# Kernel tuning notes

Hardware: AMD Instinct MI355X
Metric: run time of the kernel (lower is better)

The kernel has to match this reference:

```python
import jax, jax.numpy as jnp
from jax import lax
import numpy as np

CHUNK = 64      # chunk_size init kwarg
MAX_LOG = 20.0  # clamp bound used in ssd()
DT_BIAS = 0.01
NEG_SLOPE = 0.01  # torch LeakyReLU default


def segsum(a):
    """a: (..., T) -> (..., T, T); ss[i,j] = sum_{k=j+1..i} a[k], -inf above diag."""
    T = a.shape[-1]
    rep = jnp.broadcast_to(a[..., :, None], a.shape + (T,))
    strict_lower = jnp.tril(jnp.ones((T, T), dtype=bool), -1)
    ss = jnp.cumsum(jnp.where(strict_lower, rep, 0.0), axis=-2)
    keep = jnp.tril(jnp.ones((T, T), dtype=bool), 0)
    return jnp.where(keep, ss, -jnp.inf)


def setup_inputs() -> dict:
    key = jax.random.key(0)
    ks = jax.random.split(key, 7)
    T, B, S, F = 4096, 4, 16, 64   # time, batch, spatial heads, in_channels
    N, P, K = 16, 64, 5            # state_dim, head_dim, conv_size
    CH = 2 * N + P + 1             # bc_conv out channels = 97
    return {
        "x": jax.random.normal(ks[0], (T, B, S, F), dtype=jnp.float32),
        "conv_w": jax.random.normal(ks[1], (CH, F, K), dtype=jnp.float32) * 0.05,
        "conv_b": jax.random.normal(ks[2], (CH,), dtype=jnp.float32) * 0.05,
        "pass_w": jax.random.normal(ks[3], (1, F), dtype=jnp.float32) * 0.1,
        "pass_b": jax.random.normal(ks[4], (1,), dtype=jnp.float32) * 0.1,
        "red_w": jax.random.normal(ks[5], (1, P), dtype=jnp.float32) * 0.1,
        "red_b": jax.random.normal(ks[6], (1,), dtype=jnp.float32) * 0.1,
        "dt_param": jnp.zeros((1,), dtype=jnp.float32),  # torch init [0.0]
    }


def _forward(x, conv_w, conv_b, pass_w, pass_b, red_w, red_b, dt_param):
    T, B, S, F = x.shape
    CH, _, K = conv_w.shape
    P = red_w.shape[1]
    N = (CH - P - 1) // 2
    c = T // CHUNK

    # ---- _compute_ssm_params (parallel mode, causal left-pad) ----
    xr = jnp.moveaxis(x.reshape(T, B * S, F), 0, 2)          # (bs, F, T)
    xp = jnp.pad(xr, ((0, 0), (0, 0), (K - 1, 0)))           # left pad context
    bcax = lax.conv_general_dilated(
        xp, conv_w, window_strides=(1,), padding="VALID",
        dimension_numbers=("NCH", "OIH", "NCH")) + conv_b[None, :, None]
    bcax = jax.nn.sigmoid(bcax) + bcax                        # (bs, CH, T)
    bcax = bcax.reshape(B, S, CH, T)
    Bm = bcax[:, :, :N, :]                                    # (b,s,n,t)
    Cm = bcax[:, :, N:2 * N, :]                               # (b,s,n,t)
    A = -jnp.abs(bcax[:, :, 2 * N, :])                        # (b,s,t)
    Xc = bcax[:, :, 2 * N + 1:, :]                            # (b,s,p,t)
    dt = jax.nn.softplus(dt_param)[0] + DT_BIAS
    lAd = dt * A                                              # (b,s,t)
    Bd = Bm * ((jnp.exp(lAd) - 1.0) / (A + 1e-9))[:, :, None, :]
    Dx = x @ pass_w[0] + pass_b[0]                            # (t,b,s) passthrough

    # ---- ssd: chunked Mamba-2 scan ----
    Xb = jnp.moveaxis(Xc, 3, 0).swapaxes(0, 1).reshape(B, c, CHUNK, S, P)
    Bb = jnp.moveaxis(Bd, 3, 0).swapaxes(0, 1).reshape(B, c, CHUNK, S, N)
    Cb = jnp.moveaxis(Cm, 3, 0).swapaxes(0, 1).reshape(B, c, CHUNK, S, N)
    Ab = lAd.reshape(B, S, c, CHUNK)                          # (b,s,c,l)
    A_cumsum = jnp.cumsum(Ab, axis=-1)                        # (b,s,c,l)

    L = jnp.exp(jnp.clip(segsum(Ab), -MAX_LOG, MAX_LOG))      # (b,s,c,l,l)
    Y_diag = jnp.einsum("bclsn,bcmsn,bsclm,bcmsp->bclsp", Cb, Bb, L, Xb)

    decay_states = jnp.exp(jnp.clip(A_cumsum[..., -1:] - A_cumsum, -MAX_LOG, MAX_LOG))
    states = jnp.einsum("bclsn,bscl,bclsp->bcspn", Bb, decay_states, Xb)
    states = jnp.concatenate([jnp.zeros_like(states[:, :1]), states], axis=1)

    A_last = jnp.pad(A_cumsum[..., -1], ((0, 0), (0, 0), (1, 0)))  # (b,s,c+1)
    decay_chunk = jnp.exp(jnp.clip(segsum(A_last), -MAX_LOG, MAX_LOG))
    new_states = jnp.einsum("bszc,bcspn->bzspn", decay_chunk, states)
    states_c = new_states[:, :-1]                             # (b,c,s,p,n)

    state_decay_out = jnp.exp(A_cumsum)                       # (b,s,c,l), no clamp (as in source)
    Y_off = jnp.einsum("bclsn,bcspn,bscl->bclsp", Cb, states_c, state_decay_out)

    Y = (Y_diag + Y_off).reshape(B, T, S, P).swapaxes(0, 1)   # (t,b,s,p)

    # ---- reduce + leaky-relu passthrough ----
    y = Y @ red_w[0] + red_b[0]                               # (t,b,s)
    return y + jnp.where(Dx >= 0, Dx, NEG_SLOPE * Dx)


def reference(x, conv_w, conv_b, pass_w, pass_b, red_w, red_b, dt_param):
    return _forward(x, conv_w, conv_b, pass_w, pass_b, red_w, red_b, dt_param)
```

## Files before the change

### kernel.cpp

```cpp
#include <hip/hip_runtime.h>
#include <hip/hip_bf16.h>
#include <math.h>


#define Tn 4096
#define BSn 64
#define Fn 64
#define CHn 97
#define CHP 112
#define Kn 5
#define NCn 64

typedef __attribute__((ext_vector_type(8))) short bf16x8;
typedef __attribute__((ext_vector_type(4))) float f32x4;

static __device__ __forceinline__ unsigned short f2bf(float v) {
    __hip_bfloat16 b = __float2bfloat16(v);
    return *reinterpret_cast<unsigned short*>(&b);
}
static __device__ __forceinline__ float bf2f(unsigned short u) {
    unsigned v = ((unsigned)u) << 16;
    return __builtin_bit_cast(float, v);
}
static __device__ __forceinline__ float bflo(unsigned u) {
    return __builtin_bit_cast(float, u << 16);
}
static __device__ __forceinline__ float bfhi(unsigned u) {
    return __builtin_bit_cast(float, u & 0xffff0000u);
}

#define OFF_BD   0
#define OFF_CM   (OFF_BD + 4194304)
#define OFF_LAD  (OFF_CM + 4194304)
#define OFF_XQ   (OFF_LAD + 262144)
#define OFF_DL   (OFF_XQ + 262144)
#define OFF_ACS  (OFF_DL + 262144)
#define OFF_SRED (OFF_ACS + 262144)
#define OFF_CSUM (OFF_SRED + 65536)
#define OFF_SNS  (OFF_CSUM + 4096)
#define OFF_WBH  (OFF_SNS + 65536)
#define OFF_WBL  (OFF_WBH + 17920)

__global__ __launch_bounds__(256) void k_prep(const float* __restrict__ conv_w,
                                              const float* __restrict__ pass_w,
                                              unsigned short* __restrict__ wbh,
                                              unsigned short* __restrict__ wbl) {
    int idx = blockIdx.x * 256 + threadIdx.x;
    if (idx >= Kn * CHP * Fn) return;
    int f = idx & 63;
    int rest = idx >> 6;
    int ch = rest % CHP;
    int k = rest / CHP;
    float w = 0.f;
    if (ch < CHn) w = conv_w[(ch * Fn + f) * Kn + k];
    else if (ch == 97 && k == 4) w = pass_w[f];
    unsigned short hi = f2bf(w);
    wbh[idx] = hi;
    if (ch >= 32 && ch < 48)
        wbl[(k * 16 + (ch - 32)) * 64 + f] = f2bf(w - bf2f(hi));
}

__global__ __launch_bounds__(256) void k_fwd(
    const float* __restrict__ x, const unsigned short* __restrict__ wbh,
    const unsigned short* __restrict__ wbl,
    const float* __restrict__ conv_b, const float* __restrict__ pass_b,
    const float* __restrict__ red_w, const float* __restrict__ red_b,
    const float* __restrict__ dtp,
    unsigned short* __restrict__ Cm_h, float* __restrict__ Acs_ws,
    float* __restrict__ yp_ws, float* __restrict__ sred_ws,
    float* __restrict__ csum_ws) {
    const int wgid = blockIdx.x;
    const int seq = wgid >> 3;
    const int bs = seq & 63;
    const int ci = ((seq >> 6) << 3) | (wgid & 7);
    const int tid = threadIdx.x;
    const int wv = tid >> 6, lane = tid & 63;
    const int qd = lane >> 4, n = lane & 15;

    __shared__ alignas(16) unsigned char pool[19584];
    unsigned short* xsb = (unsigned short*)pool;
    unsigned short* xlo = (unsigned short*)(pool + 9792);
    float* B0  = (float*)pool;
    float* Ct  = (float*)(pool + 5120);
    float* pxl = (float*)(pool + 10240);
    float* px2 = (float*)(pool + 11264);
    float* zsh = (float*)(pool + 12288);
    float* dl  = (float*)(pool + 12544);

    const int tB = (wv == 3) ? 6 : wv + 4;
    const unsigned short* pBw = (wv == 2) ? wbl : wbh;
    const int sB = (wv == 2) ? 16 : CHP;
    const int cB = (wv == 2) ? 0 : 16 * tB;
    bf16x8 wA[10], wB[10];
#pragma unroll
    for (int s = 0; s < 10; ++s) {
        const int k = s >> 1, f0 = 32 * (s & 1) + qd * 8;
        wA[s] = *(const bf16x8*)&wbh[((k * CHP + 16 * wv + n) << 6) + f0];
        wB[s] = *(const bf16x8*)&pBw[((k * sB + cB + n) << 6) + f0];
    }

    float4 v[5];
#pragma unroll
    for (int it = 0; it < 5; ++it) {
        int idx = tid + it * 256;
        int tt = idx >> 4, fq = (idx & 15) * 4;
        int t = ci * 64 - 4 + tt;
        v[it] = (idx < 68 * 16 && t >= 0)
                    ? *(const float4*)&x[(t * 64 + bs) * 64 + fq]
                    : make_float4(0.f, 0.f, 0.f, 0.f);
    }
#pragma unroll
    for (int it = 0; it < 5; ++it) {
        int idx = tid + it * 256;
        if (idx < 68 * 16) {
            int tt = idx >> 4, fq = (idx & 15) * 4;
            ushort4 h, lo;
            h.x = f2bf(v[it].x); lo.x = f2bf(v[it].x - bf2f(h.x));
            h.y = f2bf(v[it].y); lo.y = f2bf(v[it].y - bf2f(h.y));
            h.z = f2bf(v[it].z); lo.z = f2bf(v[it].z - bf2f(h.z));
            h.w = f2bf(v[it].w); lo.w = f2bf(v[it].w - bf2f(h.w));
            *(ushort4*)&xsb[tt * 72 + fq] = h;
            *(ushort4*)&xlo[tt * 72 + fq] = lo;
        }
    }
    __syncthreads();

    f32x4 accA[4], accB[4];
#pragma unroll
    for (int rg = 0; rg < 4; ++rg) {
        accA[rg] = (f32x4){0.f, 0.f, 0.f, 0.f};
        accB[rg] = (f32x4){0.f, 0.f, 0.f, 0.f};
    }
    if (wv == 2) {
#pragma unroll
        for (int s = 0; s < 10; ++s) {
            const int k = s >> 1, f0 = 32 * (s & 1) + qd * 8;
#pragma unroll
            for (int rg = 0; rg < 4; ++rg) {
                bf16x8 av = *(const bf16x8*)&xsb[(16 * rg + n + k) * 72 + f0];
                bf16x8 al = *(const bf16x8*)&xlo[(16 * rg + n + k) * 72 + f0];
                accA[rg] = __builtin_amdgcn_mfma_f32_16x16x32_bf16(av, wA[s], accA[rg], 0, 0, 0);
                accA[rg] = __builtin_amdgcn_mfma_f32_16x16x32_bf16(al, wA[s], accA[rg], 0, 0, 0);
                accA[rg] = __builtin_amdgcn_mfma_f32_16x16x32_bf16(av, wB[s], accA[rg], 0, 0, 0);
            }
        }
    } else {
#pragma unroll
        for (int s = 0; s < 10; ++s) {
            const int k = s >> 1, f0 = 32 * (s & 1) + qd * 8;
#pragma unroll
            for (int rg = 0; rg < 4; ++rg) {
                bf16x8 av = *(const bf16x8*)&xsb[(16 * rg + n + k) * 72 + f0];
                accA[rg] = __builtin_amdgcn_mfma_f32_16x16x32_bf16(av, wA[s], accA[rg], 0, 0, 0);
                accB[rg] = __builtin_amdgcn_mfma_f32_16x16x32_bf16(av, wB[s], accB[rg], 0, 0, 0);
            }
        }
    }
    __syncthreads();

    const int cbase = (bs * 64 + ci) * 64;
    float px[4][4];
#pragma unroll
    for (int rg = 0; rg < 4; ++rg)
#pragma unroll
        for (int reg = 0; reg < 4; ++reg) px[rg][reg] = 0.f;

    if (wv == 0) {
        const float cb0 = conv_b[n];
        const float cb4 = conv_b[64 + n], rw4 = red_w[31 + n];
#pragma unroll
        for (int rg = 0; rg < 4; ++rg)
#pragma unroll
            for (int reg = 0; reg < 4; ++reg) {
                int row = 16 * rg + 4 * qd + reg;
                float z0 = accA[rg][reg] + cb0;
                float a0 = z0 + 1.f / (1.f + __expf(-z0));
                accA[rg][reg] = a0;
                B0[row * 20 + n] = a0;
                float z4 = accB[rg][reg] + cb4;
                px[rg][reg] = (z4 + 1.f / (1.f + __expf(-z4))) * rw4;
            }
    } else if (wv == 1) {
        const float cb1 = conv_b[16 + n];
        const float cb5 = conv_b[80 + n], rw5 = red_w[47 + n];
#pragma unroll
        for (int rg = 0; rg < 4; ++rg)
#pragma unroll
            for (int reg = 0; reg < 4; ++reg) {
                int row = 16 * rg + 4 * qd + reg;
                float z1 = accA[rg][reg] + cb1;
                float a1 = z1 + 1.f / (1.f + __expf(-z1));
                Ct[row * 20 + n] = a1;
                Cm_h[(cbase + row) * 16 + n] = f2bf(a1);
                float z5 = accB[rg][reg] + cb5;
                px[rg][reg] = (z5 + 1.f / (1.f + __expf(-z5))) * rw5;
            }
    } else if (wv == 2) {
        const float cb2 = conv_b[32 + n];
        const float rw2 = (n >= 1) ? red_w[n - 1] : 0.f;
#pragma unroll
        for (int rg = 0; rg < 4; ++rg)
#pragma unroll
            for (int reg = 0; reg < 4; ++reg) {
                int row = 16 * rg + 4 * qd + reg;
                if (n == 0) zsh[row] = accA[rg][reg];
                float z = accA[rg][reg] + cb2;
                px[rg][reg] = (z + 1.f / (1.f + __expf(-z))) * rw2;
            }
    } else {
        const float cb3 = conv_b[48 + n], rw3 = red_w[15 + n];
        const float cb6 = conv_b[96], rw6 = red_w[63];
        const float pb = pass_b[0], rb = red_b[0];
#pragma unroll
        for (int rg = 0; rg < 4; ++rg)
#pragma unroll
            for (int reg = 0; reg < 4; ++reg) {
                int row = 16 * rg + 4 * qd + reg;
                float z3 = accA[rg][reg] + cb3;
                px[rg][reg] = (z3 + 1.f / (1.f + __expf(-z3))) * rw3;
                if (n == 0) {
                    float z6 = accB[rg][reg] + cb6;
                    px[rg][reg] += (z6 + 1.f / (1.f + __expf(-z6))) * rw6;
                }
                if (n == 1) {
                    float Dx = accB[rg][reg] + pb;
                    float DL = (Dx >= 0.f) ? Dx : 0.01f * Dx;
                    dl[row] = DL + rb;
                }
            }
    }
#pragma unroll
    for (int m = 1; m < 16; m <<= 1)
#pragma unroll
        for (int rg = 0; rg < 4; ++rg)
#pragma unroll
            for (int reg = 0; reg < 4; ++reg)
                px[rg][reg] += __shfl_xor(px[rg][reg], m, 64);
    if (n == 0)
#pragma unroll
        for (int rg = 0; rg < 4; ++rg)
#pragma unroll
            for (int reg = 0; reg < 4; ++reg)
                pxl[wv * 64 + 16 * rg + 4 * qd + reg] = px[rg][reg];
    __syncthreads();

    const int l = lane;
    const float dt = log1pf(expf(dtp[0])) + 0.01f;
    float zA = zsh[l] + conv_b[32];
    float aA = zA + 1.f / (1.f + __expf(-zA));
    float An = -fabsf(aA);
    float lAd = dt * An;
    float fac = (__expf(lAd) - 1.f) / (An + 1e-9f);
    float s = lAd;
#pragma unroll
    for (int k = 1; k < 64; k <<= 1) {
        float t = __shfl_up(s, k, 64);
        if (l >= k) s += t;
    }
    const float acs_l = s;
    const float tot = __shfl(s, 63, 64);
    float xq = pxl[0 * 64 + l] + pxl[1 * 64 + l] + pxl[2 * 64 + l] + pxl[3 * 64 + l];
    const float wd = fac * xq;
    const float wsd = wd * __expf(fmaxf(tot - acs_l, -20.f));
    if (wv == 3) {
        Acs_ws[bs * Tn + ci * 64 + l] = acs_l;
        if (l == 0) csum_ws[bs * 64 + ci] = tot;
    }

    const float4 cc0 = *(const float4*)&Ct[l * 20 + 0];
    const float4 cc1 = *(const float4*)&Ct[l * 20 + 4];
    const float4 cc2 = *(const float4*)&Ct[l * 20 + 8];
    const float4 cc3 = *(const float4*)&Ct[l * 20 + 12];
    float part = 0.f;
#pragma unroll
    for (int mm = 0; mm < 16; ++mm) {
        const int m = 16 * wv + mm;
        const float4 b0 = *(const float4*)&B0[m * 20 + 0];
        const float4 b1 = *(const float4*)&B0[m * 20 + 4];
        const float4 b2 = *(const float4*)&B0[m * 20 + 8];
        const float4 b3 = *(const float4*)&B0[m * 20 + 12];
        float g = cc0.x * b0.x + cc0.y * b0.y + cc0.z * b0.z + cc0.w * b0.w +
                  cc1.x * b1.x + cc1.y * b1.y + cc1.z * b1.z + cc1.w * b1.w +
                  cc2.x * b2.x + cc2.y * b2.y + cc2.z * b2.z + cc2.w * b2.w +
                  cc3.x * b3.x + cc3.y * b3.y + cc3.z * b3.z + cc3.w * b3.w;
        float am = __shfl(acs_l, m, 64);
        float wm = __shfl(wd, m, 64);
        float arg = (m <= l) ? fmaxf(acs_l - am, -20.f) : -20.f;
        part += __expf(arg) * g * wm;
    }
    px2[wv * 64 + l] = part;

    if (wv == 0) {
        float sp = 0.f;
#pragma unroll
        for (int rg = 0; rg < 4; ++rg)
#pragma unroll
            for (int reg = 0; reg < 4; ++reg)
                sp += accA[rg][reg] * __shfl(wsd, 16 * rg + 4 * qd + reg, 64);
        sp += __shfl_xor(sp, 16, 64);
        sp += __shfl_xor(sp, 32, 64);
        if (l < 16) sred_ws[(bs * 64 + ci) * 16 + l] = sp;
    }
    __syncthreads();

    if (wv == 0)
        yp_ws[bs * Tn + ci * 64 + l] =
            px2[0 * 64 + l] + px2[1 * 64 + l] + px2[2 * 64 + l] + px2[3 * 64 + l] + dl[l];
}

__global__ __launch_bounds__(256) void k_out(
    const unsigned short* __restrict__ Cm_h, const float* __restrict__ Acs_ws,
    const float* __restrict__ sred_ws, const float* __restrict__ csum_ws,
    const float* __restrict__ yp_ws, float* __restrict__ out) {
    const int bs = blockIdx.y;
    const int tid = threadIdx.x;
    const int wv = tid >> 6, l = tid & 63;
    const int ci = blockIdx.x * 4 + wv;
    __shared__ float sn[4][16];
    const int base = bs * Tn + ci * 64;

    const float dexp = __expf(csum_ws[bs * 64 + l]);
#pragma unroll
    for (int j = 0; j < 4; ++j) {
        const int n = 4 * wv + j;
        float s = sred_ws[(bs * 64 + l) * 16 + n];
        float d = dexp;
#pragma unroll
        for (int k = 1; k < 64; k <<= 1) {
            float dp = __shfl_up(d, k, 64);
            float sp = __shfl_up(s, k, 64);
            if (l >= k) {
                s = d * sp + s;
                d = d * dp;
            }
        }
        float se = __shfl_up(s, 1, 64);
        float sns = (l == 0) ? 0.f : se;
        if ((l >> 2) == blockIdx.x) sn[l & 3][n] = sns;
    }

    const unsigned short* crow = &Cm_h[((bs * 64 + ci) * 64 + l) * 16];
    uint4 ua = *(const uint4*)crow;
    uint4 ub = *(const uint4*)(crow + 8);
    float yp = yp_ws[base + l];
    float acl = Acs_ws[base + l];
    __syncthreads();

    const float* s = sn[wv];
    float go = bflo(ua.x) * s[0]  + bfhi(ua.x) * s[1] +
               bflo(ua.y) * s[2]  + bfhi(ua.y) * s[3] +
               bflo(ua.z) * s[4]  + bfhi(ua.z) * s[5] +
               bflo(ua.w) * s[6]  + bfhi(ua.w) * s[7] +
               bflo(ub.x) * s[8]  + bfhi(ub.x) * s[9] +
               bflo(ub.y) * s[10] + bfhi(ub.y) * s[11] +
               bflo(ub.z) * s[12] + bfhi(ub.z) * s[13] +
               bflo(ub.w) * s[14] + bfhi(ub.w) * s[15];
    out[(ci * 64 + l) * 64 + bs] = yp + __expf(acl) * go;
}

extern "C" void kernel_launch(void* const* d_in, const int* in_sizes, int n_in,
                              void* d_out, int out_size, void* d_ws,
                              size_t ws_size, hipStream_t stream) {
    const float* x = (const float*)d_in[0];
    const float* conv_w = (const float*)d_in[1];
    const float* conv_b = (const float*)d_in[2];
    const float* pass_w = (const float*)d_in[3];
    const float* pass_b = (const float*)d_in[4];
    const float* red_w = (const float*)d_in[5];
    const float* red_b = (const float*)d_in[6];
    const float* dtp = (const float*)d_in[7];
    float* out = (float*)d_out;
    float* W = (float*)d_ws;
    (void)in_sizes; (void)n_in; (void)out_size; (void)ws_size;

    unsigned short* Cm_h = (unsigned short*)(W + OFF_CM);
    float* yp_ws = W + OFF_DL;
    float* Acs_ws = W + OFF_ACS;
    float* sred_ws = W + OFF_SRED;
    float* csum_ws = W + OFF_CSUM;
    unsigned short* wbh = (unsigned short*)(W + OFF_WBH);
    unsigned short* wbl = (unsigned short*)(W + OFF_WBL);

    k_prep<<<dim3((Kn * CHP * Fn + 255) / 256), dim3(256), 0, stream>>>(
        conv_w, pass_w, wbh, wbl);
    k_fwd<<<dim3(NCn * BSn), dim3(256), 0, stream>>>(
        x, wbh, wbl, conv_b, pass_b, red_w, red_b, dtp,
        Cm_h, Acs_ws, yp_ws, sred_ws, csum_ws);
    k_out<<<dim3(NCn / 4, BSn), dim3(256), 0, stream>>>(
        Cm_h, Acs_ws, sred_ws, csum_ws, yp_ws, out);
}
```

Measured before the change: 199.6 us.

## Make k_fwd persistent over 8 tiles with register prefetch of next x tile

The forward kernel now launches 512 blocks, and each loops over 8 consecutive (bs, chunk) tiles instead of launching one block per tile. Each block loads its weight fragments into registers once and reuses them across the 8 tiles. It also issues the global loads for the next tile's x slice right after the MFMA stage, so they overlap with the epilogue math. The cost is fewer blocks, which lowers occupancy and latency hiding, and an extra barrier per tile. The tile-to-block mapping also changes from the old interleaved ordering to contiguous bs runs, which can affect L2 reuse of the overlapping x halos.

```diff
diff --git a/kernel.cpp b/kernel.cpp
--- a/kernel.cpp
+++ b/kernel.cpp
@@ -10,6 +10,8 @@
 #define CHP 112
 #define Kn 5
 #define NCn 64
+#define NBLK 512
+#define TPB 8
 
 typedef __attribute__((ext_vector_type(8))) short bf16x8;
 typedef __attribute__((ext_vector_type(4))) float f32x4;
@@ -69,10 +71,7 @@
     unsigned short* __restrict__ Cm_h, float* __restrict__ Acs_ws,
     float* __restrict__ yp_ws, float* __restrict__ sred_ws,
     float* __restrict__ csum_ws) {
-    const int wgid = blockIdx.x;
-    const int seq = wgid >> 3;
-    const int bs = seq & 63;
-    const int ci = ((seq >> 6) << 3) | (wgid & 7);
+    const int b = blockIdx.x;
     const int tid = threadIdx.x;
     const int wv = tid >> 6, lane = tid & 63;
     const int qd = lane >> 4, n = lane & 15;
@@ -99,213 +98,239 @@
         wB[s] = *(const bf16x8*)&pBw[((k * sB + cB + n) << 6) + f0];
     }
 
+    const float dt = log1pf(expf(dtp[0])) + 0.01f;
+
     float4 v[5];
-#pragma unroll
-    for (int it = 0; it < 5; ++it) {
-        int idx = tid + it * 256;
-        int tt = idx >> 4, fq = (idx & 15) * 4;
-        int t = ci * 64 - 4 + tt;
-        v[it] = (idx < 68 * 16 && t >= 0)
-                    ? *(const float4*)&x[(t * 64 + bs) * 64 + fq]
-                    : make_float4(0.f, 0.f, 0.f, 0.f);
+    {
+        const int t0 = b * TPB;
+        const int bs = t0 & 63, ci = t0 >> 6;
+#pragma unroll
+        for (int it = 0; it < 5; ++it) {
+            int idx = tid + it * 256;
+            int tt = idx >> 4, fq = (idx & 15) * 4;
+            int t = ci * 64 - 4 + tt;
+            v[it] = (idx < 68 * 16 && t >= 0)
+                        ? *(const float4*)&x[(t * 64 + bs) * 64 + fq]
+                        : make_float4(0.f, 0.f, 0.f, 0.f);
+        }
     }
-#pragma unroll
-    for (int it = 0; it < 5; ++it) {
-        int idx = tid + it * 256;
-        if (idx < 68 * 16) {
-            int tt = idx >> 4, fq = (idx & 15) * 4;
-            ushort4 h, lo;
-            h.x = f2bf(v[it].x); lo.x = f2bf(v[it].x - bf2f(h.x));
-            h.y = f2bf(v[it].y); lo.y = f2bf(v[it].y - bf2f(h.y));
-            h.z = f2bf(v[it].z); lo.z = f2bf(v[it].z - bf2f(h.z));
-            h.w = f2bf(v[it].w); lo.w = f2bf(v[it].w - bf2f(h.w));
-            *(ushort4*)&xsb[tt * 72 + fq] = h;
-            *(ushort4*)&xlo[tt * 72 + fq] = lo;
-        }
+
+    for (int it8 = 0; it8 < TPB; ++it8) {
+        const int tt8 = b * TPB + it8;
+        const int bs = tt8 & 63, ci = tt8 >> 6;
+
+#pragma unroll
+        for (int it = 0; it < 5; ++it) {
+            int idx = tid + it * 256;
+            if (idx < 68 * 16) {
+                int tt = idx >> 4, fq = (idx & 15) * 4;
+                ushort4 h, lo;
+                h.x = f2bf(v[it].x); lo.x = f2bf(v[it].x - bf2f(h.x));
+                h.y = f2bf(v[it].y); lo.y = f2bf(v[it].y - bf2f(h.y));
+                h.z = f2bf(v[it].z); lo.z = f2bf(v[it].z - bf2f(h.z));
+                h.w = f2bf(v[it].w); lo.w = f2bf(v[it].w - bf2f(h.w));
+                *(ushort4*)&xsb[tt * 72 + fq] = h;
+                *(ushort4*)&xlo[tt * 72 + fq] = lo;
+            }
+        }
+        __syncthreads();
+
+        f32x4 accA[4], accB[4];
+#pragma unroll
+        for (int rg = 0; rg < 4; ++rg) {
+            accA[rg] = (f32x4){0.f, 0.f, 0.f, 0.f};
+            accB[rg] = (f32x4){0.f, 0.f, 0.f, 0.f};
+        }
+        if (wv == 2) {
+#pragma unroll
+            for (int s = 0; s < 10; ++s) {
+                const int k = s >> 1, f0 = 32 * (s & 1) + qd * 8;
+#pragma unroll
+                for (int rg = 0; rg < 4; ++rg) {
+                    bf16x8 av = *(const bf16x8*)&xsb[(16 * rg + n + k) * 72 + f0];
+                    bf16x8 al = *(const bf16x8*)&xlo[(16 * rg + n + k) * 72 + f0];
+                    accA[rg] = __builtin_amdgcn_mfma_f32_16x16x32_bf16(av, wA[s], accA[rg], 0, 0, 0);
+                    accA[rg] = __builtin_amdgcn_mfma_f32_16x16x32_bf16(al, wA[s], accA[rg], 0, 0, 0);
+                    accA[rg] = __builtin_amdgcn_mfma_f32_16x16x32_bf16(av, wB[s], accA[rg], 0, 0, 0);
+                }
+            }
+        } else {
+#pragma unroll
+            for (int s = 0; s < 10; ++s) {
+                const int k = s >> 1, f0 = 32 * (s & 1) + qd * 8;
+#pragma unroll
+                for (int rg = 0; rg < 4; ++rg) {
+                    bf16x8 av = *(const bf16x8*)&xsb[(16 * rg + n + k) * 72 + f0];
+                    accA[rg] = __builtin_amdgcn_mfma_f32_16x16x32_bf16(av, wA[s], accA[rg], 0, 0, 0);
+                    accB[rg] = __builtin_amdgcn_mfma_f32_16x16x32_bf16(av, wB[s], accB[rg], 0, 0, 0);
+                }
+            }
+        }
+        __syncthreads();
+
+        if (it8 + 1 < TPB) {
+            const int tn = tt8 + 1;
+            const int bsN = tn & 63, ciN = tn >> 6;
+#pragma unroll
+            for (int it = 0; it < 5; ++it) {
+                int idx = tid + it * 256;
+                int tt = idx >> 4, fq = (idx & 15) * 4;
+                int t = ciN * 64 - 4 + tt;
+                v[it] = (idx < 68 * 16 && t >= 0)
+                            ? *(const float4*)&x[(t * 64 + bsN) * 64 + fq]
+                            : make_float4(0.f, 0.f, 0.f, 0.f);
+            }
+        }
+
+        const int cbase = (bs * 64 + ci) * 64;
+        float px[4][4];
+#pragma unroll
+        for (int rg = 0; rg < 4; ++rg)
+#pragma unroll
+            for (int reg = 0; reg < 4; ++reg) px[rg][reg] = 0.f;
+
+        if (wv == 0) {
+            const float cb0 = conv_b[n];
+            const float cb4 = conv_b[64 + n], rw4 = red_w[31 + n];
+#pragma unroll
+            for (int rg = 0; rg < 4; ++rg)
+#pragma unroll
+                for (int reg = 0; reg < 4; ++reg) {
+                    int row = 16 * rg + 4 * qd + reg;
+                    float z0 = accA[rg][reg] + cb0;
+                    float a0 = z0 + 1.f / (1.f + __expf(-z0));
+                    accA[rg][reg] = a0;
+                    B0[row * 20 + n] = a0;
+                    float z4 = accB[rg][reg] + cb4;
+                    px[rg][reg] = (z4 + 1.f / (1.f + __expf(-z4))) * rw4;
+                }
+        } else if (wv == 1) {
+            const float cb1 = conv_b[16 + n];
+            const float cb5 = conv_b[80 + n], rw5 = red_w[47 + n];
+#pragma unroll
+            for (int rg = 0; rg < 4; ++rg)
+#pragma unroll
+                for (int reg = 0; reg < 4; ++reg) {
+                    int row = 16 * rg + 4 * qd + reg;
+                    float z1 = accA[rg][reg] + cb1;
+                    float a1 = z1 + 1.f / (1.f + __expf(-z1));
+                    Ct[row * 20 + n] = a1;
+                    Cm_h[(cbase + row) * 16 + n] = f2bf(a1);
+                    float z5 = accB[rg][reg] + cb5;
+                    px[rg][reg] = (z5 + 1.f / (1.f + __expf(-z5))) * rw5;
+                }
+        } else if (wv == 2) {
+            const float cb2 = conv_b[32 + n];
+            const float rw2 = (n >= 1) ? red_w[n - 1] : 0.f;
+#pragma unroll
+            for (int rg = 0; rg < 4; ++rg)
+#pragma unroll
+                for (int reg = 0; reg < 4; ++reg) {
+                    int row = 16 * rg + 4 * qd + reg;
+                    if (n == 0) zsh[row] = accA[rg][reg];
+                    float z = accA[rg][reg] + cb2;
+                    px[rg][reg] = (z + 1.f / (1.f + __expf(-z))) * rw2;
+                }
+        } else {
+            const float cb3 = conv_b[48 + n], rw3 = red_w[15 + n];
+            const float cb6 = conv_b[96], rw6 = red_w[63];
+            const float pb = pass_b[0], rb = red_b[0];
+#pragma unroll
+            for (int rg = 0; rg < 4; ++rg)
+#pragma unroll
+                for (int reg = 0; reg < 4; ++reg) {
+                    int row = 16 * rg + 4 * qd + reg;
+                    float z3 = accA[rg][reg] + cb3;
+                    px[rg][reg] = (z3 + 1.f / (1.f + __expf(-z3))) * rw3;
+                    if (n == 0) {
+                        float z6 = accB[rg][reg] + cb6;
+                        px[rg][reg] += (z6 + 1.f / (1.f + __expf(-z6))) * rw6;
+                    }
+                    if (n == 1) {
+                        float Dx = accB[rg][reg] + pb;
+                        float DL = (Dx >= 0.f) ? Dx : 0.01f * Dx;
+                        dl[row] = DL + rb;
+                    }
+                }
+        }
+#pragma unroll
+        for (int m = 1; m < 16; m <<= 1)
+#pragma unroll
+            for (int rg = 0; rg < 4; ++rg)
+#pragma unroll
+                for (int reg = 0; reg < 4; ++reg)
+                    px[rg][reg] += __shfl_xor(px[rg][reg], m, 64);
+        if (n == 0)
+#pragma unroll
+            for (int rg = 0; rg < 4; ++rg)
+#pragma unroll
+                for (int reg = 0; reg < 4; ++reg)
+                    pxl[wv * 64 + 16 * rg + 4 * qd + reg] = px[rg][reg];
+        __syncthreads();
+
+        const int l = lane;
+        float zA = zsh[l] + conv_b[32];
+        float aA = zA + 1.f / (1.f + __expf(-zA));
+        float An = -fabsf(aA);
+        float lAd = dt * An;
+        float fac = (__expf(lAd) - 1.f) / (An + 1e-9f);
+        float s = lAd;
+#pragma unroll
+        for (int k = 1; k < 64; k <<= 1) {
+            float t2 = __shfl_up(s, k, 64);
+            if (l >= k) s += t2;
+        }
+        const float acs_l = s;
+        const float tot = __shfl(s, 63, 64);
+        float xq = pxl[0 * 64 + l] + pxl[1 * 64 + l] + pxl[2 * 64 + l] + pxl[3 * 64 + l];
+        const float wd = fac * xq;
+        const float wsd = wd * __expf(fmaxf(tot - acs_l, -20.f));
+        if (wv == 3) {
+            Acs_ws[bs * Tn + ci * 64 + l] = acs_l;
+            if (l == 0) csum_ws[bs * 64 + ci] = tot;
+        }
+
+        if (wv == 0) {
+            float sp = 0.f;
+#pragma unroll
+            for (int rg = 0; rg < 4; ++rg)
+#pragma unroll
+                for (int reg = 0; reg < 4; ++reg)
+                    sp += accA[rg][reg] * __shfl(wsd, 16 * rg + 4 * qd + reg, 64);
+            sp += __shfl_xor(sp, 16, 64);
+            sp += __shfl_xor(sp, 32, 64);
+            if (l < 16) sred_ws[(bs * 64 + ci) * 16 + l] = sp;
+        }
+
+        const float4 cc0 = *(const float4*)&Ct[l * 20 + 0];
+        const float4 cc1 = *(const float4*)&Ct[l * 20 + 4];
+        const float4 cc2 = *(const float4*)&Ct[l * 20 + 8];
+        const float4 cc3 = *(const float4*)&Ct[l * 20 + 12];
+        float part = 0.f;
+#pragma unroll
+        for (int mm = 0; mm < 16; ++mm) {
+            const int m = 16 * wv + mm;
+            const float4 b0 = *(const float4*)&B0[m * 20 + 0];
+            const float4 b1 = *(const float4*)&B0[m * 20 + 4];
+            const float4 b2 = *(const float4*)&B0[m * 20 + 8];
+            const float4 b3 = *(const float4*)&B0[m * 20 + 12];
+            float g = cc0.x * b0.x + cc0.y * b0.y + cc0.z * b0.z + cc0.w * b0.w +
+                      cc1.x * b1.x + cc1.y * b1.y + cc1.z * b1.z + cc1.w * b1.w +
+                      cc2.x * b2.x + cc2.y * b2.y + cc2.z * b2.z + cc2.w * b2.w +
+                      cc3.x * b3.x + cc3.y * b3.y + cc3.z * b3.z + cc3.w * b3.w;
+            float am = __shfl(acs_l, m, 64);
+            float wm = __shfl(wd, m, 64);
+            float arg = (m <= l) ? fmaxf(acs_l - am, -20.f) : -20.f;
+            part += __expf(arg) * g * wm;
+        }
+        px2[wv * 64 + l] = part;
+        __syncthreads();
+
+        if (wv == 0)
+            yp_ws[bs * Tn + ci * 64 + l] =
+                px2[0 * 64 + l] + px2[1 * 64 + l] + px2[2 * 64 + l] + px2[3 * 64 + l] + dl[l];
+        __syncthreads();
     }
-    __syncthreads();
-
-    f32x4 accA[4], accB[4];
-#pragma unroll
-    for (int rg = 0; rg < 4; ++rg) {
-        accA[rg] = (f32x4){0.f, 0.f, 0.f, 0.f};
-        accB[rg] = (f32x4){0.f, 0.f, 0.f, 0.f};
-    }
-    if (wv == 2) {
-#pragma unroll
-        for (int s = 0; s < 10; ++s) {
-            const int k = s >> 1, f0 = 32 * (s & 1) + qd * 8;
-#pragma unroll
-            for (int rg = 0; rg < 4; ++rg) {
-                bf16x8 av = *(const bf16x8*)&xsb[(16 * rg + n + k) * 72 + f0];
-                bf16x8 al = *(const bf16x8*)&xlo[(16 * rg + n + k) * 72 + f0];
-                accA[rg] = __builtin_amdgcn_mfma_f32_16x16x32_bf16(av, wA[s], accA[rg], 0, 0, 0);
-                accA[rg] = __builtin_amdgcn_mfma_f32_16x16x32_bf16(al, wA[s], accA[rg], 0, 0, 0);
-                accA[rg] = __builtin_amdgcn_mfma_f32_16x16x32_bf16(av, wB[s], accA[rg], 0, 0, 0);
-            }
-        }
-    } else {
-#pragma unroll
-        for (int s = 0; s < 10; ++s) {
-            const int k = s >> 1, f0 = 32 * (s & 1) + qd * 8;
-#pragma unroll
-            for (int rg = 0; rg < 4; ++rg) {
-                bf16x8 av = *(const bf16x8*)&xsb[(16 * rg + n + k) * 72 + f0];
-                accA[rg] = __builtin_amdgcn_mfma_f32_16x16x32_bf16(av, wA[s], accA[rg], 0, 0, 0);
-                accB[rg] = __builtin_amdgcn_mfma_f32_16x16x32_bf16(av, wB[s], accB[rg], 0, 0, 0);
-            }
-        }
-    }
-    __syncthreads();
-
-    const int cbase = (bs * 64 + ci) * 64;
-    float px[4][4];
-#pragma unroll
-    for (int rg = 0; rg < 4; ++rg)
-#pragma unroll
-        for (int reg = 0; reg < 4; ++reg) px[rg][reg] = 0.f;
-
-    if (wv == 0) {
-        const float cb0 = conv_b[n];
-        const float cb4 = conv_b[64 + n], rw4 = red_w[31 + n];
-#pragma unroll
-        for (int rg = 0; rg < 4; ++rg)
-#pragma unroll
-            for (int reg = 0; reg < 4; ++reg) {
-                int row = 16 * rg + 4 * qd + reg;
-                float z0 = accA[rg][reg] + cb0;
-                float a0 = z0 + 1.f / (1.f + __expf(-z0));
-                accA[rg][reg] = a0;
-                B0[row * 20 + n] = a0;
-                float z4 = accB[rg][reg] + cb4;
-                px[rg][reg] = (z4 + 1.f / (1.f + __expf(-z4))) * rw4;
-            }
-    } else if (wv == 1) {
-        const float cb1 = conv_b[16 + n];
-        const float cb5 = conv_b[80 + n], rw5 = red_w[47 + n];
-#pragma unroll
-        for (int rg = 0; rg < 4; ++rg)
-#pragma unroll
-            for (int reg = 0; reg < 4; ++reg) {
-                int row = 16 * rg + 4 * qd + reg;
-                float z1 = accA[rg][reg] + cb1;
-                float a1 = z1 + 1.f / (1.f + __expf(-z1));
-                Ct[row * 20 + n] = a1;
-                Cm_h[(cbase + row) * 16 + n] = f2bf(a1);
-                float z5 = accB[rg][reg] + cb5;
-                px[rg][reg] = (z5 + 1.f / (1.f + __expf(-z5))) * rw5;
-            }
-    } else if (wv == 2) {
-        const float cb2 = conv_b[32 + n];
-        const float rw2 = (n >= 1) ? red_w[n - 1] : 0.f;
-#pragma unroll
-        for (int rg = 0; rg < 4; ++rg)
-#pragma unroll
-            for (int reg = 0; reg < 4; ++reg) {
-                int row = 16 * rg + 4 * qd + reg;
-                if (n == 0) zsh[row] = accA[rg][reg];
-                float z = accA[rg][reg] + cb2;
-                px[rg][reg] = (z + 1.f / (1.f + __expf(-z))) * rw2;
-            }
-    } else {
-        const float cb3 = conv_b[48 + n], rw3 = red_w[15 + n];
-        const float cb6 = conv_b[96], rw6 = red_w[63];
-        const float pb = pass_b[0], rb = red_b[0];
-#pragma unroll
-        for (int rg = 0; rg < 4; ++rg)
-#pragma unroll
-            for (int reg = 0; reg < 4; ++reg) {
-                int row = 16 * rg + 4 * qd + reg;
-                float z3 = accA[rg][reg] + cb3;
-                px[rg][reg] = (z3 + 1.f / (1.f + __expf(-z3))) * rw3;
-                if (n == 0) {
-                    float z6 = accB[rg][reg] + cb6;
-                    px[rg][reg] += (z6 + 1.f / (1.f + __expf(-z6))) * rw6;
-                }
-                if (n == 1) {
-                    float Dx = accB[rg][reg] + pb;
-                    float DL = (Dx >= 0.f) ? Dx : 0.01f * Dx;
-                    dl[row] = DL + rb;
-                }
-            }
-    }
-#pragma unroll
-    for (int m = 1; m < 16; m <<= 1)
-#pragma unroll
-        for (int rg = 0; rg < 4; ++rg)
-#pragma unroll
-            for (int reg = 0; reg < 4; ++reg)
-                px[rg][reg] += __shfl_xor(px[rg][reg], m, 64);
-    if (n == 0)
-#pragma unroll
-        for (int rg = 0; rg < 4; ++rg)
-#pragma unroll
-            for (int reg = 0; reg < 4; ++reg)
-                pxl[wv * 64 + 16 * rg + 4 * qd + reg] = px[rg][reg];
-    __syncthreads();
-
-    const int l = lane;
-    const float dt = log1pf(expf(dtp[0])) + 0.01f;
-    float zA = zsh[l] + conv_b[32];
-    float aA = zA + 1.f / (1.f + __expf(-zA));
-    float An = -fabsf(aA);
-    float lAd = dt * An;
-    float fac = (__expf(lAd) - 1.f) / (An + 1e-9f);
-    float s = lAd;
-#pragma unroll
-    for (int k = 1; k < 64; k <<= 1) {
-        float t = __shfl_up(s, k, 64);
-        if (l >= k) s += t;
-    }
-    const float acs_l = s;
-    const float tot = __shfl(s, 63, 64);
-    float xq = pxl[0 * 64 + l] + pxl[1 * 64 + l] + pxl[2 * 64 + l] + pxl[3 * 64 + l];
-    const float wd = fac * xq;
-    const float wsd = wd * __expf(fmaxf(tot - acs_l, -20.f));
-    if (wv == 3) {
-        Acs_ws[bs * Tn + ci * 64 + l] = acs_l;
-        if (l == 0) csum_ws[bs * 64 + ci] = tot;
-    }
-
-    const float4 cc0 = *(const float4*)&Ct[l * 20 + 0];
-    const float4 cc1 = *(const float4*)&Ct[l * 20 + 4];
-    const float4 cc2 = *(const float4*)&Ct[l * 20 + 8];
-    const float4 cc3 = *(const float4*)&Ct[l * 20 + 12];
-    float part = 0.f;
-#pragma unroll
-    for (int mm = 0; mm < 16; ++mm) {
-        const int m = 16 * wv + mm;
-        const float4 b0 = *(const float4*)&B0[m * 20 + 0];
-        const float4 b1 = *(const float4*)&B0[m * 20 + 4];
-        const float4 b2 = *(const float4*)&B0[m * 20 + 8];
-        const float4 b3 = *(const float4*)&B0[m * 20 + 12];
-        float g = cc0.x * b0.x + cc0.y * b0.y + cc0.z * b0.z + cc0.w * b0.w +
-                  cc1.x * b1.x + cc1.y * b1.y + cc1.z * b1.z + cc1.w * b1.w +
-                  cc2.x * b2.x + cc2.y * b2.y + cc2.z * b2.z + cc2.w * b2.w +
-                  cc3.x * b3.x + cc3.y * b3.y + cc3.z * b3.z + cc3.w * b3.w;
-        float am = __shfl(acs_l, m, 64);
-        float wm = __shfl(wd, m, 64);
-        float arg = (m <= l) ? fmaxf(acs_l - am, -20.f) : -20.f;
-        part += __expf(arg) * g * wm;
-    }
-    px2[wv * 64 + l] = part;
-
-    if (wv == 0) {
-        float sp = 0.f;
-#pragma unroll
-        for (int rg = 0; rg < 4; ++rg)
-#pragma unroll
-            for (int reg = 0; reg < 4; ++reg)
-                sp += accA[rg][reg] * __shfl(wsd, 16 * rg + 4 * qd + reg, 64);
-        sp += __shfl_xor(sp, 16, 64);
-        sp += __shfl_xor(sp, 32, 64);
-        if (l < 16) sred_ws[(bs * 64 + ci) * 16 + l] = sp;
-    }
-    __syncthreads();
-
-    if (wv == 0)
-        yp_ws[bs * Tn + ci * 64 + l] =
-            px2[0 * 64 + l] + px2[1 * 64 + l] + px2[2 * 64 + l] + px2[3 * 64 + l] + dl[l];
 }
 
 __global__ __launch_bounds__(256) void k_out(
@@ -383,7 +408,7 @@
 
     k_prep<<<dim3((Kn * CHP * Fn + 255) / 256), dim3(256), 0, stream>>>(
         conv_w, pass_w, wbh, wbl);
-    k_fwd<<<dim3(NCn * BSn), dim3(256), 0, stream>>>(
+    k_fwd<<<dim3(NBLK), dim3(256), 0, stream>>>(
         x, wbh, wbl, conv_b, pass_b, red_w, red_b, dtp,
         Cm_h, Acs_ws, yp_ws, sred_ws, csum_ws);
     k_out<<<dim3(NCn / 4, BSn), dim3(256), 0, stream>>>(
```

Result: slower. 229.4 us (+14.9%).
